# Kernel optimization log

Hardware: AMD Instinct MI355X
Metric: run time of the kernel (lower is better)

Reference implementation:

```python
import jax, jax.numpy as jnp
import numpy as np

B, C, D, H, W = 2, 32, 96, 96, 96
RED = 16
INV_SQRT2 = 0.7071067811865476  # 1/sqrt(2), Haar analysis filter coefficient
BN_EPS = 1e-5


def _haar1(x, axis):
    # pywt 'haar' DWT on even-length signals: a[i]=(x[2i]+x[2i+1])/sqrt2, d[i]=(x[2i]-x[2i+1])/sqrt2
    e = jax.lax.slice_in_dim(x, 0, None, stride=2, axis=axis)
    o = jax.lax.slice_in_dim(x, 1, None, stride=2, axis=axis)
    return (e + o) * INV_SQRT2, (e - o) * INV_SQRT2


def haar_dwt3d(x):
    # x: (B, C, D, H, W). Separable 3D Haar DWT; key letters follow pywt dwtn
    # axis order (D, H, W): 'aad' = approx along D, approx along H, detail along W.
    aD, dD = _haar1(x, 2)
    aa, ad = _haar1(aD, 3)
    da, dd = _haar1(dD, 3)
    aaa, aad = _haar1(aa, 4)
    ada, add = _haar1(ad, 4)
    daa, dad = _haar1(da, 4)
    dda, ddd = _haar1(dd, 4)
    # per-channel grouping of 7 detail bands, then flatten to (B, 7C, D/2, H/2, W/2)
    high = jnp.stack([aad, ada, add, daa, dad, dda, ddd], axis=2)
    b, c = x.shape[0], x.shape[1]
    high = high.reshape(b, c * 7, *aaa.shape[2:])
    return aaa, high


def chan_attn(x, w1, w2):
    # AdaptiveAvgPool3d(1) -> FC(no bias) -> ReLU -> FC(no bias) -> Sigmoid -> scale
    y = x.mean(axis=(2, 3, 4))                     # (B, Ch)
    y = jax.nn.sigmoid(jnp.maximum(y @ w1.T, 0.0) @ w2.T)
    return x * y[:, :, None, None, None]


def setup_inputs() -> dict:
    key = jax.random.key(0)
    ks = jax.random.split(key, 7)
    x = jax.random.normal(ks[0], (B, C, D, H, W), dtype=jnp.float32)
    w1_low = jax.random.normal(ks[1], (C // RED, C), dtype=jnp.float32) * 0.1
    w2_low = jax.random.normal(ks[2], (C, C // RED), dtype=jnp.float32) * 0.1
    w1_high = jax.random.normal(ks[3], (7 * C // RED, 7 * C), dtype=jnp.float32) * 0.05
    w2_high = jax.random.normal(ks[4], (7 * C, 7 * C // RED), dtype=jnp.float32) * 0.05
    w_fuse = jax.random.normal(ks[5], (C, 8 * C), dtype=jnp.float32) * 0.05  # 1x1x1 conv kernel
    b_fuse = jnp.zeros((C,), dtype=jnp.float32)
    gamma = jnp.ones((C,), dtype=jnp.float32)
    beta = jnp.zeros((C,), dtype=jnp.float32)
    return dict(x=x, w1_low=w1_low, w2_low=w2_low, w1_high=w1_high, w2_high=w2_high,
                w_fuse=w_fuse, b_fuse=b_fuse, gamma=gamma, beta=beta)


def reference(x, w1_low, w2_low, w1_high, w2_high, w_fuse, b_fuse, gamma, beta):
    low, high = haar_dwt3d(x)                                  # (B,C,48,48,48), (B,7C,48,48,48)
    low = chan_attn(low, w1_low, w2_low)
    high = chan_attn(high, w1_high, w2_high)
    z = jnp.concatenate([low, high], axis=1)                   # (B, 8C, 48,48,48)
    z = jnp.einsum('bcdhw,oc->bodhw', z, w_fuse) + b_fuse[None, :, None, None, None]
    # BatchNorm3d (training-mode batch statistics, as fresh torch module defaults)
    mu = z.mean(axis=(0, 2, 3, 4), keepdims=True)
    var = z.var(axis=(0, 2, 3, 4), keepdims=True)
    z = (z - mu) * jax.lax.rsqrt(var + BN_EPS)
    z = z * gamma[None, :, None, None, None] + beta[None, :, None, None, None]
    return jnp.maximum(z, 0.0)
```

## Files before the change

kernel.cpp:

```cpp
#include <hip/hip_runtime.h>
#include <math.h>

#define HS 0.35355339059327373f
#define NSPAT 110592
#define NBN   221184

__global__ __launch_bounds__(256) void k1_parity(const float* __restrict__ x,
                                                 float* __restrict__ S) {
    int blk = blockIdx.x;
    int d   = blk % 96;
    int bc  = blk / 96;
    const float4* x4 = (const float4*)x + (long)blk * 2304;
    int tid = threadIdx.x;
    float aE0 = 0.f, aO0 = 0.f, aE1 = 0.f, aO1 = 0.f;
#pragma unroll
    for (int i = 0; i < 9; ++i) {
        int f = tid + i * 256;
        float4 v = x4[f];
        int h = f / 24;
        float e = v.x + v.z, o = v.y + v.w;
        if (h & 1) { aE1 += e; aO1 += o; }
        else       { aE0 += e; aO0 += o; }
    }
#pragma unroll
    for (int m = 32; m; m >>= 1) {
        aE0 += __shfl_xor(aE0, m, 64); aO0 += __shfl_xor(aO0, m, 64);
        aE1 += __shfl_xor(aE1, m, 64); aO1 += __shfl_xor(aO1, m, 64);
    }
    __shared__ float red[4][4];
    int lane = tid & 63, wave = tid >> 6;
    if (lane == 0) { red[wave][0] = aE0; red[wave][1] = aO0;
                     red[wave][2] = aE1; red[wave][3] = aO1; }
    __syncthreads();
    if (tid < 4) {
        float v = red[0][tid] + red[1][tid] + red[2][tid] + red[3][tid];
        int q = tid >> 1, r = tid & 1, p = d & 1;
        atomicAdd(&S[bc * 8 + p * 4 + q * 2 + r], v);
    }
}

__global__ __launch_bounds__(256) void k2_attn(
        const float* __restrict__ S,
        const float* __restrict__ w1l, const float* __restrict__ w2l,
        const float* __restrict__ w1h, const float* __restrict__ w2h,
        const float* __restrict__ wf, float* __restrict__ A) {
    int b = blockIdx.x, tid = threadIdx.x;
    __shared__ float mlow[32], mhigh[224], h1l[2], h1h[14], ylow[32], yhigh[224];
    const float* Sb = S + b * 256;
    const float MS = HS / (float)NSPAT;
    if (tid < 32) {
        float s = 0.f;
        for (int j = 0; j < 8; ++j) s += Sb[tid * 8 + j];
        mlow[tid] = s * MS;
    }
    if (tid < 224) {
        int c = tid / 7, k = tid % 7, dm = k + 1;
        float s = 0.f;
        for (int j = 0; j < 8; ++j) {
            float sg = (__popc(j & dm) & 1) ? -1.f : 1.f;
            s += sg * Sb[c * 8 + j];
        }
        mhigh[tid] = s * MS;
    }
    __syncthreads();
    if (tid < 2) {
        float s = 0.f;
        for (int c = 0; c < 32; ++c) s += w1l[tid * 32 + c] * mlow[c];
        h1l[tid] = fmaxf(s, 0.f);
    } else if (tid < 16) {
        int j = tid - 2;
        float s = 0.f;
        for (int c = 0; c < 224; ++c) s += w1h[j * 224 + c] * mhigh[c];
        h1h[j] = fmaxf(s, 0.f);
    }
    __syncthreads();
    if (tid < 32) {
        float s = w2l[tid * 2] * h1l[0] + w2l[tid * 2 + 1] * h1l[1];
        ylow[tid] = 1.f / (1.f + expf(-s));
    } else if (tid < 256) {
        int i = tid - 32;
        float s = 0.f;
        for (int j = 0; j < 14; ++j) s += w2h[i * 14 + j] * h1h[j];
        yhigh[i] = 1.f / (1.f + expf(-s));
    }
    __syncthreads();
    for (int idx = tid; idx < 8192; idx += 256) {
        int o = idx >> 8, c = (idx >> 3) & 31, pqr = idx & 7;
        float a = wf[o * 256 + c] * ylow[c];
#pragma unroll
        for (int k = 0; k < 7; ++k) {
            float sg = (__popc(pqr & (k + 1)) & 1) ? -1.f : 1.f;
            a += sg * wf[o * 256 + 32 + c * 7 + k] * yhigh[c * 7 + k];
        }
        int og = o >> 3, op = o & 7;
        A[b * 8192 + og * 2048 + c * 64 + op * 8 + pqr] = a * HS;
    }
}

__global__ __launch_bounds__(256) void k3_main(const float* __restrict__ x,
                                               const float* __restrict__ A,
                                               float* __restrict__ z,
                                               float* __restrict__ bnRep) {
    int blk  = blockIdx.x;
    int vblk = blk % 36;
    int tmp  = blk / 36;
    int od   = tmp % 48;
    int b    = tmp / 48;
    int tid  = threadIdx.x;
    int lane = tid & 63;
    int wv   = __builtin_amdgcn_readfirstlane(tid >> 6);
    int v    = vblk * 64 + lane;
    int oh   = v / 48, ow = v % 48;

    const float* Ab = A + b * 8192 + wv * 2048;

    float acc[8];
#pragma unroll
    for (int o = 0; o < 8; ++o) acc[o] = 0.f;

    const float2* x2 = (const float2*)x;
    int base = (b * 32) * 442368 + od * 9216 + oh * 96 + ow;

    float2 v00 = x2[base],        v01 = x2[base + 48];
    float2 v10 = x2[base + 4608], v11 = x2[base + 4656];
    for (int c = 0; c < 32; ++c) {
        float2 n00, n01, n10, n11;
        if (c < 31) {
            int nb = base + (c + 1) * 442368;
            n00 = x2[nb];        n01 = x2[nb + 48];
            n10 = x2[nb + 4608]; n11 = x2[nb + 4656];
        }
        const float* Ac = Ab + c * 64;
#pragma unroll
        for (int o = 0; o < 8; ++o) {
            const float* Ao = Ac + o * 8;
            acc[o] += Ao[0] * v00.x + Ao[1] * v00.y + Ao[2] * v01.x + Ao[3] * v01.y
                    + Ao[4] * v10.x + Ao[5] * v10.y + Ao[6] * v11.x + Ao[7] * v11.y;
        }
        v00 = n00; v01 = n01; v10 = n10; v11 = n11;
    }

#pragma unroll
    for (int o = 0; o < 8; ++o) {
        z[((b * 32 + wv * 8 + o) * 48 + od) * 2304 + v] = acc[o];
    }

    int rep = (blockIdx.x & 15) * 64;
#pragma unroll
    for (int o = 0; o < 8; ++o) {
        float sv = acc[o];
        float qv = acc[o] * acc[o];
#pragma unroll
        for (int m = 32; m; m >>= 1) {
            sv += __shfl_xor(sv, m, 64);
            qv += __shfl_xor(qv, m, 64);
        }
        if (lane == 0) {
            atomicAdd(&bnRep[rep + wv * 8 + o], sv);
            atomicAdd(&bnRep[rep + 32 + wv * 8 + o], qv);
        }
    }
}

__global__ __launch_bounds__(256) void k5_norm(float* __restrict__ z,
                                               const float* __restrict__ bnRep,
                                               const float* __restrict__ gamma,
                                               const float* __restrict__ beta) {
    __shared__ float s_sc[32], s_sh[32];
    int tid = threadIdx.x;
    if (tid < 32) {
        float s = 0.f, q = 0.f;
#pragma unroll
        for (int r = 0; r < 16; ++r) {
            s += bnRep[r * 64 + tid];
            q += bnRep[r * 64 + 32 + tid];
        }
        const float invN = 1.f / (float)NBN;
        float mean = s * invN;
        float var  = q * invN - mean * mean;
        float inv  = rsqrtf(var + 1e-5f);
        float sc   = gamma[tid] * inv;
        s_sc[tid] = sc;
        s_sh[tid] = beta[tid] - mean * sc;
    }
    int i = blockIdx.x * 256 + tid;
    float4* z4 = (float4*)z;
    float4 v = z4[i];
    __syncthreads();
    int o = (i / 27648) & 31;
    float sc = s_sc[o], sh = s_sh[o];
    v.x = fmaxf(v.x * sc + sh, 0.f);
    v.y = fmaxf(v.y * sc + sh, 0.f);
    v.z = fmaxf(v.z * sc + sh, 0.f);
    v.w = fmaxf(v.w * sc + sh, 0.f);
    z4[i] = v;
}

extern "C" void kernel_launch(void* const* d_in, const int* in_sizes, int n_in,
                              void* d_out, int out_size, void* d_ws, size_t ws_size,
                              hipStream_t stream) {
    const float* x    = (const float*)d_in[0];
    const float* w1l  = (const float*)d_in[1];
    const float* w2l  = (const float*)d_in[2];
    const float* w1h  = (const float*)d_in[3];
    const float* w2h  = (const float*)d_in[4];
    const float* wf   = (const float*)d_in[5];
    const float* gamma = (const float*)d_in[7];
    const float* beta  = (const float*)d_in[8];
    float* out = (float*)d_out;

    float* ws    = (float*)d_ws;
    float* S     = ws;
    float* bnRep = ws + 512;
    float* A     = ws + 2048;

    hipMemsetAsync(d_ws, 0, 1536 * sizeof(float), stream);
    k1_parity<<<6144, 256, 0, stream>>>(x, S);
    k2_attn<<<2, 256, 0, stream>>>(S, w1l, w2l, w1h, w2h, wf, A);
    k3_main<<<3456, 256, 0, stream>>>(x, A, out, bnRep);
    k5_norm<<<6912, 256, 0, stream>>>(out, bnRep, gamma, beta);
}
```

Before: 469.9 us.

## Share input loads across waves via double-buffered LDS in main conv kernel

Each wave now loads only its own (d,h) parity slice of the input for 8 channels at a time and writes it into a double-buffered shared-memory tile. All four waves then read all four slices from LDS. This removes the 4x redundant global loads of the same input values across waves and batches more loads in flight. In exchange it adds block-level barriers, extra register staging and LDS traffic.

```diff
diff --git a/kernel.cpp b/kernel.cpp
--- a/kernel.cpp
+++ b/kernel.cpp
@@ -101,6 +101,7 @@
                                                const float* __restrict__ A,
                                                float* __restrict__ z,
                                                float* __restrict__ bnRep) {
+    __shared__ float2 buf[2][8][4][64];
     int blk  = blockIdx.x;
     int vblk = blk % 36;
     int tmp  = blk / 36;
@@ -112,32 +113,49 @@
     int v    = vblk * 64 + lane;
     int oh   = v / 48, ow = v % 48;
 
+    int p = wv >> 1, q = wv & 1;
+    const float2* x2 = (const float2*)x;
+    int gbase = (b * 32) * 442368 + (2 * od + p) * 4608 + (2 * oh + q) * 48 + ow;
+
     const float* Ab = A + b * 8192 + wv * 2048;
 
     float acc[8];
 #pragma unroll
     for (int o = 0; o < 8; ++o) acc[o] = 0.f;
 
-    const float2* x2 = (const float2*)x;
-    int base = (b * 32) * 442368 + od * 9216 + oh * 96 + ow;
-
-    float2 v00 = x2[base],        v01 = x2[base + 48];
-    float2 v10 = x2[base + 4608], v11 = x2[base + 4656];
-    for (int c = 0; c < 32; ++c) {
-        float2 n00, n01, n10, n11;
-        if (c < 31) {
-            int nb = base + (c + 1) * 442368;
-            n00 = x2[nb];        n01 = x2[nb + 48];
-            n10 = x2[nb + 4608]; n11 = x2[nb + 4656];
-        }
-        const float* Ac = Ab + c * 64;
-#pragma unroll
-        for (int o = 0; o < 8; ++o) {
-            const float* Ao = Ac + o * 8;
-            acc[o] += Ao[0] * v00.x + Ao[1] * v00.y + Ao[2] * v01.x + Ao[3] * v01.y
-                    + Ao[4] * v10.x + Ao[5] * v10.y + Ao[6] * v11.x + Ao[7] * v11.y;
-        }
-        v00 = n00; v01 = n01; v10 = n10; v11 = n11;
+    float2 st[8];
+#pragma unroll
+    for (int i = 0; i < 8; ++i) st[i] = x2[gbase + i * 442368];
+#pragma unroll
+    for (int i = 0; i < 8; ++i) buf[0][i][wv][lane] = st[i];
+    __syncthreads();
+
+    for (int cc = 0; cc < 4; ++cc) {
+        if (cc < 3) {
+#pragma unroll
+            for (int i = 0; i < 8; ++i)
+                st[i] = x2[gbase + ((cc + 1) * 8 + i) * 442368];
+        }
+#pragma unroll
+        for (int i = 0; i < 8; ++i) {
+            float2 v00 = buf[cc & 1][i][0][lane];
+            float2 v01 = buf[cc & 1][i][1][lane];
+            float2 v10 = buf[cc & 1][i][2][lane];
+            float2 v11 = buf[cc & 1][i][3][lane];
+            const float* Ac = Ab + (cc * 8 + i) * 64;
+#pragma unroll
+            for (int o = 0; o < 8; ++o) {
+                const float* Ao = Ac + o * 8;
+                acc[o] += Ao[0] * v00.x + Ao[1] * v00.y + Ao[2] * v01.x + Ao[3] * v01.y
+                        + Ao[4] * v10.x + Ao[5] * v10.y + Ao[6] * v11.x + Ao[7] * v11.y;
+            }
+        }
+        if (cc < 3) {
+            __syncthreads();
+#pragma unroll
+            for (int i = 0; i < 8; ++i) buf[(cc + 1) & 1][i][wv][lane] = st[i];
+            __syncthreads();
+        }
     }
 
 #pragma unroll
```

Result: slower. 661.3 us (+40.7%).
